# Kernel tuning notes

Measured on AMD Instinct MI355X. Metric: run time of the kernel, lower is better.

## Reference

```python
import jax, jax.numpy as jnp
import numpy as np

B = 4096   # batch
NC = 1     # input channels
K1 = 30    # layer-1 channels
K2 = 80    # layer-2 channels
P = 3      # pooling window (p_x = p_y = 3)
H = 28     # input spatial size (forced: 28 -> conv8 -> 21 -> pool3 -> 7 -> conv4 -> 4)


def _conv(x, w):
    # torch Conv2d (valid, stride 1, no bias): x NCHW, w OIHW
    return jax.lax.conv_general_dilated(x, w, (1, 1), 'VALID',
                                        dimension_numbers=('NCHW', 'OIHW', 'NCHW'))


def _conv_t(x, w):
    # torch ConvTranspose2d (stride 1, no pad, no bias). w: [in, out, kh, kw].
    # Equivalent to full cross-correlation with spatially-flipped, channel-swapped kernel.
    k = w.shape[2]
    wf = jnp.flip(w, (2, 3)).transpose(1, 0, 2, 3)  # -> OIHW
    return jax.lax.conv_general_dilated(x, wf, (1, 1), [(k - 1, k - 1), (k - 1, k - 1)],
                                        dimension_numbers=('NCHW', 'OIHW', 'NCHW'))


def setup_inputs() -> dict:
    key = jax.random.key(0)
    ks = jax.random.split(key, 12)
    sc = 0.05
    f32 = jnp.float32
    return {
        'x':        jax.random.normal(ks[0], (B, NC, H, H), f32),
        'enc1_w':   jax.random.normal(ks[1], (K1, NC, 8, 8), f32) * sc,   # Conv2d OIHW
        'pool_w1':  jax.random.normal(ks[2], (9, 9), f32) * sc,           # Linear [out,in], no bias
        'pool_w2':  jax.random.normal(ks[3], (9, 9), f32) * sc,
        'enc2_w':   jax.random.normal(ks[4], (K2, K1, 4, 4), f32) * sc,
        'h_w':      jax.random.normal(ks[5], (K2, 16, 16), f32) * sc,     # stacked Linear(16,16) [out,in]
        'h_b':      jnp.zeros((K2, 16), f32),
        'mean_w':   jax.random.normal(ks[6], (K2, 16, 16), f32) * sc,
        'mean_b':   jnp.zeros((K2, 16), f32),
        'logvar_w': jax.random.normal(ks[7], (K2, 16, 16), f32) * sc,
        'logvar_b': jnp.zeros((K2, 16), f32),
        'dec2_w':   jax.random.normal(ks[8], (K2, K1, 4, 4), f32) * sc,   # ConvTranspose [in,out,kh,kw]
        'dec1_w':   jax.random.normal(ks[9], (K1, NC, 8, 8), f32) * sc,
        'alpha':    jnp.asarray(0.5, f32),
    }


def reference(x, enc1_w, pool_w1, pool_w2, enc2_w, h_w, h_b,
              mean_w, mean_b, logvar_w, logvar_b, dec2_w, dec1_w, alpha):
    k_pool, k_unpool, k_code, k_noise = jax.random.split(jax.random.key(42), 4)

    # --- encoder conv 1 ---
    c1 = _conv(x, enc1_w)                               # [B, K1, 21, 21]
    b, c, hp, wp = c1.shape
    n, m = hp // P, wp // P                             # 7, 7

    # --- stochastic pooling (vectorized over B, K1, n, m tiles) ---
    tiles = c1.reshape(b, c, n, P, m, P).transpose(0, 1, 2, 4, 3, 5)
    tiles = tiles.reshape(b, c, n, m, P * P)            # [B,K1,7,7,9]
    h1 = jnp.tanh(jnp.einsum('bcnmt,ot->bcnmo', tiles, pool_w1))
    eta = jax.nn.softmax(jnp.einsum('bcnmt,ot->bcnmo', h1, pool_w2), axis=-1)
    zeta = jax.random.categorical(k_pool, jnp.log(eta))  # [B,K1,7,7]
    pooled = jnp.take_along_axis(tiles, zeta[..., None], axis=-1)[..., 0]  # [B,K1,7,7]

    # --- encoder conv 2 + per-channel code MLPs ---
    c2 = _conv(pooled, enc2_w)                          # [B, K2, 4, 4]
    flat = c2.reshape(b, K2, 16)                        # [B, K2, 16]
    h = jnp.tanh(jnp.einsum('bki,koi->bko', flat, h_w) + h_b)
    mean = jnp.einsum('bki,koi->bko', h, mean_w) + mean_b      # [B,K2,16]
    log_var = jnp.einsum('bki,koi->bko', h, logvar_w) + logvar_b

    # --- reparameterized sample per channel ---
    std = jnp.exp(0.5 * log_var)
    s = (mean + std * jax.random.normal(k_code, mean.shape, mean.dtype)).reshape(c2.shape)

    # --- decoder ---
    s2 = _conv_t(s, dec2_w)                             # [B, K1, 7, 7]

    # stochastic unpooling: fresh multinomial draw from the same etas, scatter into tile
    zeta2 = jax.random.categorical(k_unpool, jnp.log(eta))      # [B,K1,7,7]
    tiles_u = jax.nn.one_hot(zeta2, P * P, dtype=s2.dtype) * s2[..., None]  # [B,K1,7,7,9]
    s1 = tiles_u.reshape(b, c, n, m, P, P).transpose(0, 1, 2, 4, 3, 5).reshape(b, c, n * P, m * P)
    s1 = _conv_t(s1, dec1_w)                            # [B, NC, 28, 28]

    # --- add_noise: std = (1/alpha) * eye(H, W), zero std off-diagonal ---
    noise_std = (1.0 / alpha) * jnp.eye(s1.shape[-2], s1.shape[-1], dtype=s1.dtype)
    x_rec = s1 + noise_std * jax.random.normal(k_noise, s1.shape, s1.dtype)

    return x_rec, mean, log_var, eta
```

## Files before the change

kernel.cpp:

```cpp
#include <hip/hip_runtime.h>
#include <cstdint>


#define OFF_MEAN 3211264
#define OFF_LV   8454144
#define OFF_ETA  13697024

constexpr uint64_t ctf(uint32_t k0, uint32_t k1, uint32_t x0, uint32_t x1) {
  uint32_t ks0 = k0, ks1 = k1, ks2 = k0 ^ k1 ^ 0x1BD11BDAu;
  const int rotA[4] = {13, 15, 26, 6};
  const int rotB[4] = {17, 29, 16, 24};
  x0 += ks0; x1 += ks1;
  for (int g = 0; g < 5; ++g) {
    for (int i = 0; i < 4; ++i) {
      int r = (g & 1) ? rotB[i] : rotA[i];
      x0 += x1;
      x1 = (uint32_t)((x1 << r) | (x1 >> (32 - r)));
      x1 ^= x0;
    }
    uint32_t ka = (g + 1) % 3 == 0 ? ks0 : ((g + 1) % 3 == 1 ? ks1 : ks2);
    uint32_t kb = (g + 2) % 3 == 0 ? ks0 : ((g + 2) % 3 == 1 ? ks1 : ks2);
    x0 += ka;
    x1 += kb + (uint32_t)(g + 1);
  }
  return ((uint64_t)x0 << 32) | (uint64_t)x1;
}

constexpr uint64_t KP_ = ctf(0u, 42u, 0u, 0u);
constexpr uint64_t KU_ = ctf(0u, 42u, 0u, 1u);
constexpr uint64_t KC_ = ctf(0u, 42u, 0u, 2u);
constexpr uint64_t KN_ = ctf(0u, 42u, 0u, 3u);
constexpr uint32_t KPOOL0 = (uint32_t)(KP_ >> 32), KPOOL1 = (uint32_t)KP_;
constexpr uint32_t KUNP0  = (uint32_t)(KU_ >> 32), KUNP1  = (uint32_t)KU_;
constexpr uint32_t KCODE0 = (uint32_t)(KC_ >> 32), KCODE1 = (uint32_t)KC_;
constexpr uint32_t KNOIS0 = (uint32_t)(KN_ >> 32), KNOIS1 = (uint32_t)KN_;

__device__ __forceinline__ uint2 tf_dev(uint32_t k0, uint32_t k1, uint32_t x0, uint32_t x1) {
  uint32_t ks2 = k0 ^ k1 ^ 0x1BD11BDAu;
  x0 += k0; x1 += k1;
#define TFR(r) { x0 += x1; x1 = (x1 << (r)) | (x1 >> (32 - (r))); x1 ^= x0; }
  TFR(13) TFR(15) TFR(26) TFR(6)
  x0 += k1;  x1 += ks2 + 1u;
  TFR(17) TFR(29) TFR(16) TFR(24)
  x0 += ks2; x1 += k0 + 2u;
  TFR(13) TFR(15) TFR(26) TFR(6)
  x0 += k0;  x1 += k1 + 3u;
  TFR(17) TFR(29) TFR(16) TFR(24)
  x0 += k1;  x1 += ks2 + 4u;
  TFR(13) TFR(15) TFR(26) TFR(6)
  x0 += ks2; x1 += k0 + 5u;
#undef TFR
  return make_uint2(x0, x1);
}

__device__ __forceinline__ uint32_t rbits32(uint32_t k0, uint32_t k1, uint32_t idx) {
  uint2 r = tf_dev(k0, k1, 0u, idx);
  return r.x ^ r.y;
}

__device__ __forceinline__ float u01_from_bits(uint32_t bits) {
  return __uint_as_float((bits >> 9) | 0x3F800000u) - 1.0f;
}

__device__ __forceinline__ float gumbel_draw(uint32_t k0, uint32_t k1, uint32_t idx) {
  float u01 = u01_from_bits(rbits32(k0, k1, idx));
  float u = fmaxf(__fadd_rn(u01, 1.17549435e-38f), 1.17549435e-38f);
  return -logf(-logf(u));
}

__device__ __forceinline__ float erfinv_xla(float x) {
  float t = __fmul_rn(x, x);
  float w = -log1pf(-t);
  float p;
  if (w < 5.0f) {
    w = __fadd_rn(w, -2.5f);
    p = 2.81022636e-08f;
    p = __fadd_rn(__fmul_rn(p, w), 3.43273939e-07f);
    p = __fadd_rn(__fmul_rn(p, w), -3.5233877e-06f);
    p = __fadd_rn(__fmul_rn(p, w), -4.39150654e-06f);
    p = __fadd_rn(__fmul_rn(p, w), 0.00021858087f);
    p = __fadd_rn(__fmul_rn(p, w), -0.00125372503f);
    p = __fadd_rn(__fmul_rn(p, w), -0.00417768164f);
    p = __fadd_rn(__fmul_rn(p, w), 0.246640727f);
    p = __fadd_rn(__fmul_rn(p, w), 1.50140941f);
  } else {
    w = __fadd_rn(sqrtf(w), -3.0f);
    p = -0.000200214257f;
    p = __fadd_rn(__fmul_rn(p, w), 0.000100950558f);
    p = __fadd_rn(__fmul_rn(p, w), 0.00134934322f);
    p = __fadd_rn(__fmul_rn(p, w), -0.00367342844f);
    p = __fadd_rn(__fmul_rn(p, w), 0.00573950773f);
    p = __fadd_rn(__fmul_rn(p, w), -0.0076224613f);
    p = __fadd_rn(__fmul_rn(p, w), 0.00943887047f);
    p = __fadd_rn(__fmul_rn(p, w), 1.00167406f);
    p = __fadd_rn(__fmul_rn(p, w), 2.83297682f);
  }
  return __fmul_rn(p, x);
}

__device__ __forceinline__ float normal_draw(uint32_t k0, uint32_t k1, uint32_t idx) {
  float u01 = u01_from_bits(rbits32(k0, k1, idx));
  float u = fmaxf(__fadd_rn(__fmul_rn(u01, 2.0f), -0.99999994f), -0.99999994f);
  return __fmul_rn(1.41421356237309515f, erfinv_xla(u));
}

__device__ __forceinline__ float tanh_xla(float x) {
  float ax = fabsf(x);
  float xc = fmaxf(fminf(x, 7.90531110763549805f), -7.90531110763549805f);
  float x2 = __fmul_rn(xc, xc);
  float p = __fmaf_rn(x2, -2.76076847742355e-16f, 2.00018790482477e-13f);
  p = __fmaf_rn(x2, p, -8.60467152213735e-11f);
  p = __fmaf_rn(x2, p, 5.12229709037114e-08f);
  p = __fmaf_rn(x2, p, 1.48572235717979e-05f);
  p = __fmaf_rn(x2, p, 6.37261928875436e-04f);
  p = __fmaf_rn(x2, p, 4.89352455891786e-03f);
  p = __fmul_rn(xc, p);
  float q = __fmaf_rn(x2, 1.19825839466702e-06f, 1.18534705686654e-04f);
  q = __fmaf_rn(x2, q, 2.26843463243900e-03f);
  q = __fmaf_rn(x2, q, 4.89352518554385e-03f);
  return (ax < 0.0004f) ? x : __fdiv_rn(p, q);
}

__global__ __launch_bounds__(256) void k_enc(
    const float* __restrict__ x, const float* __restrict__ enc1_w,
    const float* __restrict__ pw1, const float* __restrict__ pw2,
    const float* __restrict__ enc2_w, const float* __restrict__ h_w,
    const float* __restrict__ h_b, const float* __restrict__ mean_w,
    const float* __restrict__ mean_b, const float* __restrict__ lv_w,
    const float* __restrict__ lv_b,
    float* __restrict__ o_mean, float* __restrict__ o_lv, float* __restrict__ o_eta,
    float* __restrict__ ws_s, unsigned char* __restrict__ ws_z) {
  __shared__ float lds[2866];
  __shared__ float pooled[1470];
  const int b = blockIdx.x, tid = threadIdx.x;

  float* xs  = lds;
  float* w1s = lds + 784;
  float* pp1 = lds + 2704;
  float* pp2 = lds + 2785;
  for (int i = tid; i < 784; i += 256) xs[i] = x[(size_t)b * 784 + i];
  for (int i = tid; i < 1920; i += 256) w1s[i] = enc1_w[i];
  if (tid < 81) { pp1[tid] = pw1[tid]; pp2[tid] = pw2[tid]; }
  __syncthreads();

  for (int g = tid; g < 1470; g += 256) {
    const int c = g / 49, cell = g - c * 49;
    const int n = cell / 7, m = cell - n * 7;
    const int yb = n * 3, xb = m * 3;
    const float* wc = &w1s[c * 64];

    float R[3][10];
#pragma unroll
    for (int rr = 0; rr < 3; ++rr)
#pragma unroll
      for (int i = 0; i < 10; ++i) R[rr][i] = xs[(yb + rr) * 28 + xb + i];

    float tile[9];
#pragma unroll
    for (int i = 0; i < 9; ++i) tile[i] = 0.f;

#pragma unroll
    for (int dy = 0; dy < 8; ++dy) {
      float4 wa = *(const float4*)&wc[dy * 8];
      float4 wb = *(const float4*)&wc[dy * 8 + 4];
      float w8[8] = {wa.x, wa.y, wa.z, wa.w, wb.x, wb.y, wb.z, wb.w};
#pragma unroll
      for (int dx = 0; dx < 8; ++dx) {
        float w = w8[dx];
#pragma unroll
        for (int p = 0; p < 3; ++p)
#pragma unroll
          for (int q = 0; q < 3; ++q)
            tile[p * 3 + q] = __fmaf_rn(R[(dy + p) % 3][dx + q], w, tile[p * 3 + q]);
      }
      if (dy < 7) {
#pragma unroll
        for (int i = 0; i < 10; ++i) R[dy % 3][i] = xs[(yb + dy + 3) * 28 + xb + i];
      }
    }

    float h1v[9];
#pragma unroll
    for (int o = 0; o < 9; ++o) {
      float a = 0.f;
#pragma unroll
      for (int t = 0; t < 9; ++t) a += tile[t] * pp1[o * 9 + t];
      h1v[o] = tanh_xla(a);
    }
    float lg[9], mx = -3.4e38f;
#pragma unroll
    for (int o = 0; o < 9; ++o) {
      float a = 0.f;
#pragma unroll
      for (int t = 0; t < 9; ++t) a += h1v[t] * pp2[o * 9 + t];
      lg[o] = a;
      mx = fmaxf(mx, a);
    }
    float ev[9], ssum = 0.f;
#pragma unroll
    for (int o = 0; o < 9; ++o) { ev[o] = expf(__fadd_rn(lg[o], -mx)); ssum += ev[o]; }
    float leta[9];
    size_t ebase = ((size_t)(b * 30 + c) * 49 + cell) * 9;
#pragma unroll
    for (int o = 0; o < 9; ++o) {
      float e = __fdiv_rn(ev[o], ssum);
      o_eta[ebase + o] = e;
      leta[o] = logf(e);
    }
    uint32_t fb = (uint32_t)ebase;
    float best1 = -3.4e38f, best2 = -3.4e38f, pooledv = 0.f;
    int z2 = 0;
#pragma unroll
    for (int t = 0; t < 9; ++t) {
      float v1 = __fadd_rn(leta[t], gumbel_draw(KPOOL0, KPOOL1, fb + t));
      bool t1 = v1 > best1; best1 = t1 ? v1 : best1; pooledv = t1 ? tile[t] : pooledv;
      float v2 = __fadd_rn(leta[t], gumbel_draw(KUNP0, KUNP1, fb + t));
      bool t2 = v2 > best2; best2 = t2 ? v2 : best2; z2 = t2 ? t : z2;
    }
    pooled[g] = pooledv;
    ws_z[(size_t)b * 1470 + g] = (unsigned char)z2;
  }
  __syncthreads();

  float* c2s = lds;
  float* hs  = lds + 1280;
  const int k2l = tid >> 4, pos = tid & 15;
  const int uy = pos >> 2, ux = pos & 3;
  {
    float acc[5] = {0.f, 0.f, 0.f, 0.f, 0.f};
    for (int c = 0; c < 30; ++c) {
      float pr[16];
#pragma unroll
      for (int dy = 0; dy < 4; ++dy)
#pragma unroll
        for (int dx = 0; dx < 4; ++dx)
          pr[dy * 4 + dx] = pooled[c * 49 + (uy + dy) * 7 + ux + dx];
#pragma unroll
      for (int j = 0; j < 5; ++j) {
        const float4* wr = (const float4*)&enc2_w[(size_t)((j * 16 + k2l) * 30 + c) * 16];
        float4 w0 = wr[0], w1 = wr[1], w2 = wr[2], w3 = wr[3];
        float a = acc[j];
        a = __fmaf_rn(pr[0],  w0.x, a);  a = __fmaf_rn(pr[1],  w0.y, a);
        a = __fmaf_rn(pr[2],  w0.z, a);  a = __fmaf_rn(pr[3],  w0.w, a);
        a = __fmaf_rn(pr[4],  w1.x, a);  a = __fmaf_rn(pr[5],  w1.y, a);
        a = __fmaf_rn(pr[6],  w1.z, a);  a = __fmaf_rn(pr[7],  w1.w, a);
        a = __fmaf_rn(pr[8],  w2.x, a);  a = __fmaf_rn(pr[9],  w2.y, a);
        a = __fmaf_rn(pr[10], w2.z, a);  a = __fmaf_rn(pr[11], w2.w, a);
        a = __fmaf_rn(pr[12], w3.x, a);  a = __fmaf_rn(pr[13], w3.y, a);
        a = __fmaf_rn(pr[14], w3.z, a);  a = __fmaf_rn(pr[15], w3.w, a);
        acc[j] = a;
      }
    }
#pragma unroll
    for (int j = 0; j < 5; ++j) c2s[(j * 16 + k2l) * 16 + pos] = acc[j];
  }
  __syncthreads();

#pragma unroll
  for (int j = 0; j < 5; ++j) {
    int it = tid + j * 256;
    int k2 = it >> 4;
    const float4* wr4 = (const float4*)&h_w[(size_t)it * 16];
    float4 a0 = wr4[0], a1 = wr4[1], a2 = wr4[2], a3 = wr4[3];
    float wv16[16] = {a0.x, a0.y, a0.z, a0.w, a1.x, a1.y, a1.z, a1.w,
                      a2.x, a2.y, a2.z, a2.w, a3.x, a3.y, a3.z, a3.w};
    float d = 0.f;
#pragma unroll
    for (int i = 0; i < 16; ++i) d += c2s[k2 * 16 + i] * wv16[i];
    hs[it] = tanh_xla(__fadd_rn(d, h_b[it]));
  }
  __syncthreads();

#pragma unroll
  for (int j = 0; j < 5; ++j) {
    int it = tid + j * 256;
    int k2 = it >> 4;
    const float4* wm4 = (const float4*)&mean_w[(size_t)it * 16];
    const float4* wl4 = (const float4*)&lv_w[(size_t)it * 16];
    float4 m0 = wm4[0], m1 = wm4[1], m2 = wm4[2], m3 = wm4[3];
    float4 l0 = wl4[0], l1 = wl4[1], l2 = wl4[2], l3 = wl4[3];
    float wm16[16] = {m0.x, m0.y, m0.z, m0.w, m1.x, m1.y, m1.z, m1.w,
                      m2.x, m2.y, m2.z, m2.w, m3.x, m3.y, m3.z, m3.w};
    float wl16[16] = {l0.x, l0.y, l0.z, l0.w, l1.x, l1.y, l1.z, l1.w,
                      l2.x, l2.y, l2.z, l2.w, l3.x, l3.y, l3.z, l3.w};
    float dm = 0.f, dl = 0.f;
#pragma unroll
    for (int i = 0; i < 16; ++i) {
      float hv = hs[k2 * 16 + i];
      dm += hv * wm16[i];
      dl += hv * wl16[i];
    }
    float mean = __fadd_rn(dm, mean_b[it]);
    float lv = __fadd_rn(dl, lv_b[it]);
    size_t gi = (size_t)b * 1280 + it;
    o_mean[gi] = mean;
    o_lv[gi] = lv;
    float stdv = expf(__fmul_rn(0.5f, lv));
    float z = normal_draw(KCODE0, KCODE1, (uint32_t)(b * 1280 + it));
    ws_s[gi] = __fadd_rn(mean, __fmul_rn(stdv, z));
  }
}

__global__ __launch_bounds__(256) void k_expand(const float* __restrict__ dec2_w,
                                                float* __restrict__ Wexp) {
  int idx = blockIdx.x * 256 + threadIdx.x;
  int k = idx / 1472, t = idx - k * 1472;
  int k2 = k >> 4, iy = (k >> 2) & 3, ix = k & 3;
  int c = t / 49, cell = t - c * 49;
  int u = cell / 7, v = cell - u * 7;
  int du = u - iy, dv = v - ix;
  float val = 0.f;
  if (t < 1470 && (unsigned)du < 4u && (unsigned)dv < 4u)
    val = dec2_w[((k2 * 30 + c) << 4) + (du << 2) + dv];
  Wexp[idx] = val;
}

__global__ __launch_bounds__(256) void k_gemm(const float* __restrict__ A,
                                              const float* __restrict__ Bm,
                                              float* __restrict__ C) {
  __shared__ float As[16][132];
  __shared__ float Bs[16][64];
  const int tid = threadIdx.x;
  const int n0 = blockIdx.x * 64;
  const int m0 = blockIdx.y * 128;
  const int tx = tid & 15, ty = tid >> 4;

  float acc[8][4];
#pragma unroll
  for (int i = 0; i < 8; ++i)
#pragma unroll
    for (int j = 0; j < 4; ++j) acc[i][j] = 0.f;

  const int fa_r0 = tid >> 2, fa_c = (tid & 3) << 2;
  const int fb_k = tid >> 4, fb_c = (tid & 15) << 2;

  for (int k0 = 0; k0 < 1280; k0 += 16) {
    __syncthreads();
    float4 a0 = *(const float4*)&A[(size_t)(m0 + fa_r0) * 1280 + k0 + fa_c];
    float4 a1 = *(const float4*)&A[(size_t)(m0 + 64 + fa_r0) * 1280 + k0 + fa_c];
    float4 bv = *(const float4*)&Bm[(size_t)(k0 + fb_k) * 1472 + n0 + fb_c];
    As[fa_c + 0][fa_r0] = a0.x;  As[fa_c + 1][fa_r0] = a0.y;
    As[fa_c + 2][fa_r0] = a0.z;  As[fa_c + 3][fa_r0] = a0.w;
    As[fa_c + 0][64 + fa_r0] = a1.x;  As[fa_c + 1][64 + fa_r0] = a1.y;
    As[fa_c + 2][64 + fa_r0] = a1.z;  As[fa_c + 3][64 + fa_r0] = a1.w;
    *(float4*)&Bs[fb_k][fb_c] = bv;
    __syncthreads();

#pragma unroll
    for (int kk = 0; kk < 16; ++kk) {
      float4 av0 = *(const float4*)&As[kk][ty * 8];
      float4 av1 = *(const float4*)&As[kk][ty * 8 + 4];
      float4 bv0 = *(const float4*)&Bs[kk][tx * 4];
      float am[8] = {av0.x, av0.y, av0.z, av0.w, av1.x, av1.y, av1.z, av1.w};
      float bn[4] = {bv0.x, bv0.y, bv0.z, bv0.w};
#pragma unroll
      for (int i = 0; i < 8; ++i)
#pragma unroll
        for (int j = 0; j < 4; ++j) acc[i][j] = __fmaf_rn(am[i], bn[j], acc[i][j]);
    }
  }

#pragma unroll
  for (int i = 0; i < 8; ++i) {
    size_t row = (size_t)(m0 + ty * 8 + i);
    float4 o = make_float4(acc[i][0], acc[i][1], acc[i][2], acc[i][3]);
    *(float4*)&C[row * 1472 + n0 + tx * 4] = o;
  }
}

__global__ __launch_bounds__(256) void k_unpool(
    const float* __restrict__ S2, const unsigned char* __restrict__ ws_z,
    const float* __restrict__ dec1_w, const float* __restrict__ alpha,
    float* __restrict__ o_xrec) {
  __shared__ float w1s[1920];
  __shared__ float2 tv[1470];
  const int b = blockIdx.x, tid = threadIdx.x;

  for (int i = tid; i < 1920; i += 256) w1s[i] = dec1_w[i];
#pragma unroll
  for (int j = 0; j < 6; ++j) {
    int t = tid + j * 256;
    if (t < 1470) {
      int c = t / 49, cell = t - c * 49;
      int n = cell / 7, m = cell - n * 7;
      int z = ws_z[(size_t)b * 1470 + t];
      int p = z / 3, q = z - p * 3;
      float val = S2[(size_t)b * 1472 + t];
      tv[t] = make_float2(val, __uint_as_float((uint32_t)((n * 3 + p) | ((m * 3 + q) << 8))));
    }
  }
  __syncthreads();

  float inva = __fdiv_rn(1.0f, alpha[0]);
  for (int pix = tid; pix < 784; pix += 256) {
    int y = pix / 28, x = pix - y * 28;
    int nlo = (y >= 9) ? ((y - 9 + 2) / 3) : 0;
    int nhi = min(6, y / 3);
    int mlo = (x >= 9) ? ((x - 9 + 2) / 3) : 0;
    int mhi = min(6, x / 3);

    float acc = 0.f;
    for (int c = 0; c < 30; ++c) {
      const float2* tvc = &tv[c * 49];
      const float* wc = &w1s[c * 64];
#pragma unroll
      for (int dn = 0; dn < 4; ++dn) {
        int n = nlo + dn;
        bool nok = n <= nhi;
        int nn = nok ? n : nhi;
#pragma unroll
        for (int dm = 0; dm < 4; ++dm) {
          int m = mlo + dm;
          bool ok = nok && (m <= mhi);
          int mm = (m <= mhi) ? m : mhi;
          float2 tvv = tvc[nn * 7 + mm];
          uint32_t pp = __float_as_uint(tvv.y);
          int dy = y - (int)(pp & 0xffu);
          int dx = x - (int)(pp >> 8);
          ok = ok && ((unsigned)dy < 8u) && ((unsigned)dx < 8u);
          float wvv = wc[((dy & 7) << 3) + (dx & 7)];
          acc = __fmaf_rn(ok ? tvv.x : 0.f, wvv, acc);
        }
      }
    }
    if (y == x) {
      float zn = normal_draw(KNOIS0, KNOIS1, (uint32_t)(b * 784 + pix));
      acc = __fadd_rn(acc, __fmul_rn(inva, zn));
    }
    o_xrec[(size_t)b * 784 + pix] = acc;
  }
}

extern "C" void kernel_launch(void* const* d_in, const int* in_sizes, int n_in,
                              void* d_out, int out_size, void* d_ws, size_t ws_size,
                              hipStream_t stream) {
  const float* x      = (const float*)d_in[0];
  const float* enc1_w = (const float*)d_in[1];
  const float* pw1    = (const float*)d_in[2];
  const float* pw2    = (const float*)d_in[3];
  const float* enc2_w = (const float*)d_in[4];
  const float* h_w    = (const float*)d_in[5];
  const float* h_b    = (const float*)d_in[6];
  const float* mean_w = (const float*)d_in[7];
  const float* mean_b = (const float*)d_in[8];
  const float* lv_w   = (const float*)d_in[9];
  const float* lv_b   = (const float*)d_in[10];
  const float* dec2_w = (const float*)d_in[11];
  const float* dec1_w = (const float*)d_in[12];
  const float* alpha  = (const float*)d_in[13];

  float* out = (float*)d_out;
  float* o_xrec = out;
  float* o_mean = out + OFF_MEAN;
  float* o_lv   = out + OFF_LV;
  float* o_eta  = out + OFF_ETA;

  char* wsb = (char*)d_ws;
  float* ws_s = (float*)wsb;
  unsigned char* ws_z = (unsigned char*)(wsb + 20971520);
  float* Wexp = (float*)(wsb + 26992640);
  float* S2   = (float*)(wsb + 34529280);

  k_expand<<<dim3(7360), dim3(256), 0, stream>>>(dec2_w, Wexp);
  k_enc<<<dim3(4096), dim3(256), 0, stream>>>(
      x, enc1_w, pw1, pw2, enc2_w, h_w, h_b, mean_w, mean_b, lv_w, lv_b,
      o_mean, o_lv, o_eta, ws_s, ws_z);
  k_gemm<<<dim3(23, 32), dim3(256), 0, stream>>>(ws_s, Wexp, S2);
  k_unpool<<<dim3(4096), dim3(256), 0, stream>>>(S2, ws_z, dec1_w, alpha, o_xrec);
}
```

Measured before the change: 1.690 ms.

## Retile decoder GEMM with register prefetch and process two images per unpool block

The decoder GEMM tile changes from 128x64 to 64x128, with clamped loads and a guarded store for the ragged N edge. It also prefetches the next K slice into registers while computing the current one, so global load latency overlaps the FMAs. The unpool kernel now handles two batch images per block, which amortizes the dec1 weight staging and gives each thread more pixels to work on. The trade-offs are more shared memory per unpool block and wasted work on the padded final GEMM column tile.

```diff
diff --git a/kernel.cpp b/kernel.cpp
--- a/kernel.cpp
+++ b/kernel.cpp
@@ -318,53 +318,68 @@
 __global__ __launch_bounds__(256) void k_gemm(const float* __restrict__ A,
                                               const float* __restrict__ Bm,
                                               float* __restrict__ C) {
-  __shared__ float As[16][132];
-  __shared__ float Bs[16][64];
+  __shared__ float As[16][68];
+  __shared__ float Bs[16][128];
   const int tid = threadIdx.x;
-  const int n0 = blockIdx.x * 64;
-  const int m0 = blockIdx.y * 128;
+  const int n0 = blockIdx.x * 128;
+  const int m0 = blockIdx.y * 64;
   const int tx = tid & 15, ty = tid >> 4;
 
-  float acc[8][4];
-#pragma unroll
-  for (int i = 0; i < 8; ++i)
-#pragma unroll
-    for (int j = 0; j < 4; ++j) acc[i][j] = 0.f;
-
-  const int fa_r0 = tid >> 2, fa_c = (tid & 3) << 2;
-  const int fb_k = tid >> 4, fb_c = (tid & 15) << 2;
+  float acc[4][8];
+#pragma unroll
+  for (int i = 0; i < 4; ++i)
+#pragma unroll
+    for (int j = 0; j < 8; ++j) acc[i][j] = 0.f;
+
+  const int a_r = tid >> 2, a_c = (tid & 3) << 2;
+  const int b_k = tid >> 4, b_c = (tid & 15) << 3;
+  const int bcol = n0 + b_c;
+  const int bcol_c = (bcol > 1464) ? 1464 : bcol;
+
+  const float* pa = &A[(size_t)(m0 + a_r) * 1280 + a_c];
+  const float* pb = &Bm[(size_t)b_k * 1472 + bcol_c];
+
+  float4 av = *(const float4*)pa;
+  float4 bv0 = *(const float4*)pb;
+  float4 bv1 = *(const float4*)(pb + 4);
 
   for (int k0 = 0; k0 < 1280; k0 += 16) {
     __syncthreads();
-    float4 a0 = *(const float4*)&A[(size_t)(m0 + fa_r0) * 1280 + k0 + fa_c];
-    float4 a1 = *(const float4*)&A[(size_t)(m0 + 64 + fa_r0) * 1280 + k0 + fa_c];
-    float4 bv = *(const float4*)&Bm[(size_t)(k0 + fb_k) * 1472 + n0 + fb_c];
-    As[fa_c + 0][fa_r0] = a0.x;  As[fa_c + 1][fa_r0] = a0.y;
-    As[fa_c + 2][fa_r0] = a0.z;  As[fa_c + 3][fa_r0] = a0.w;
-    As[fa_c + 0][64 + fa_r0] = a1.x;  As[fa_c + 1][64 + fa_r0] = a1.y;
-    As[fa_c + 2][64 + fa_r0] = a1.z;  As[fa_c + 3][64 + fa_r0] = a1.w;
-    *(float4*)&Bs[fb_k][fb_c] = bv;
+    As[a_c + 0][a_r] = av.x;  As[a_c + 1][a_r] = av.y;
+    As[a_c + 2][a_r] = av.z;  As[a_c + 3][a_r] = av.w;
+    *(float4*)&Bs[b_k][b_c] = bv0;
+    *(float4*)&Bs[b_k][b_c + 4] = bv1;
     __syncthreads();
 
+    if (k0 + 16 < 1280) {
+      av = *(const float4*)(pa + k0 + 16);
+      bv0 = *(const float4*)(pb + (size_t)(k0 + 16) * 1472);
+      bv1 = *(const float4*)(pb + (size_t)(k0 + 16) * 1472 + 4);
+    }
+
 #pragma unroll
     for (int kk = 0; kk < 16; ++kk) {
-      float4 av0 = *(const float4*)&As[kk][ty * 8];
-      float4 av1 = *(const float4*)&As[kk][ty * 8 + 4];
-      float4 bv0 = *(const float4*)&Bs[kk][tx * 4];
-      float am[8] = {av0.x, av0.y, av0.z, av0.w, av1.x, av1.y, av1.z, av1.w};
-      float bn[4] = {bv0.x, bv0.y, bv0.z, bv0.w};
-#pragma unroll
-      for (int i = 0; i < 8; ++i)
-#pragma unroll
-        for (int j = 0; j < 4; ++j) acc[i][j] = __fmaf_rn(am[i], bn[j], acc[i][j]);
-    }
-  }
-
-#pragma unroll
-  for (int i = 0; i < 8; ++i) {
-    size_t row = (size_t)(m0 + ty * 8 + i);
-    float4 o = make_float4(acc[i][0], acc[i][1], acc[i][2], acc[i][3]);
-    *(float4*)&C[row * 1472 + n0 + tx * 4] = o;
+      float4 a4 = *(const float4*)&As[kk][ty * 4];
+      float4 b4a = *(const float4*)&Bs[kk][tx * 8];
+      float4 b4b = *(const float4*)&Bs[kk][tx * 8 + 4];
+      float am[4] = {a4.x, a4.y, a4.z, a4.w};
+      float bn[8] = {b4a.x, b4a.y, b4a.z, b4a.w, b4b.x, b4b.y, b4b.z, b4b.w};
+#pragma unroll
+      for (int i = 0; i < 4; ++i)
+#pragma unroll
+        for (int j = 0; j < 8; ++j) acc[i][j] = __fmaf_rn(am[i], bn[j], acc[i][j]);
+    }
+  }
+
+  if (n0 + tx * 8 < 1472) {
+#pragma unroll
+    for (int i = 0; i < 4; ++i) {
+      size_t row = (size_t)(m0 + ty * 4 + i);
+      float4 o0 = make_float4(acc[i][0], acc[i][1], acc[i][2], acc[i][3]);
+      float4 o1 = make_float4(acc[i][4], acc[i][5], acc[i][6], acc[i][7]);
+      *(float4*)&C[row * 1472 + n0 + tx * 8] = o0;
+      *(float4*)&C[row * 1472 + n0 + tx * 8 + 4] = o1;
+    }
   }
 }
 
@@ -373,35 +388,38 @@
     const float* __restrict__ dec1_w, const float* __restrict__ alpha,
     float* __restrict__ o_xrec) {
   __shared__ float w1s[1920];
-  __shared__ float2 tv[1470];
-  const int b = blockIdx.x, tid = threadIdx.x;
+  __shared__ float2 tv[2][1470];
+  const int b0 = blockIdx.x * 2, tid = threadIdx.x;
 
   for (int i = tid; i < 1920; i += 256) w1s[i] = dec1_w[i];
-#pragma unroll
-  for (int j = 0; j < 6; ++j) {
-    int t = tid + j * 256;
-    if (t < 1470) {
-      int c = t / 49, cell = t - c * 49;
-      int n = cell / 7, m = cell - n * 7;
-      int z = ws_z[(size_t)b * 1470 + t];
-      int p = z / 3, q = z - p * 3;
-      float val = S2[(size_t)b * 1472 + t];
-      tv[t] = make_float2(val, __uint_as_float((uint32_t)((n * 3 + p) | ((m * 3 + q) << 8))));
-    }
+  for (int t = tid; t < 2940; t += 256) {
+    int bb = t >= 1470;
+    int tt = t - bb * 1470;
+    int c = tt / 49, cell = tt - c * 49;
+    int n = cell / 7, m = cell - n * 7;
+    int b = b0 + bb;
+    int z = ws_z[(size_t)b * 1470 + tt];
+    int p = z / 3, q = z - p * 3;
+    float val = S2[(size_t)b * 1472 + tt];
+    tv[bb][tt] = make_float2(val, __uint_as_float((uint32_t)((n * 3 + p) | ((m * 3 + q) << 8))));
   }
   __syncthreads();
 
   float inva = __fdiv_rn(1.0f, alpha[0]);
-  for (int pix = tid; pix < 784; pix += 256) {
-    int y = pix / 28, x = pix - y * 28;
+  for (int pix = tid; pix < 1568; pix += 256) {
+    int bb = pix >= 784;
+    int p2 = pix - bb * 784;
+    int b = b0 + bb;
+    int y = p2 / 28, x = p2 - y * 28;
     int nlo = (y >= 9) ? ((y - 9 + 2) / 3) : 0;
     int nhi = min(6, y / 3);
     int mlo = (x >= 9) ? ((x - 9 + 2) / 3) : 0;
     int mhi = min(6, x / 3);
 
     float acc = 0.f;
+    const float2* tvb = tv[bb];
     for (int c = 0; c < 30; ++c) {
-      const float2* tvc = &tv[c * 49];
+      const float2* tvc = &tvb[c * 49];
       const float* wc = &w1s[c * 64];
 #pragma unroll
       for (int dn = 0; dn < 4; ++dn) {
@@ -424,10 +442,10 @@
       }
     }
     if (y == x) {
-      float zn = normal_draw(KNOIS0, KNOIS1, (uint32_t)(b * 784 + pix));
+      float zn = normal_draw(KNOIS0, KNOIS1, (uint32_t)(b * 784 + p2));
       acc = __fadd_rn(acc, __fmul_rn(inva, zn));
     }
-    o_xrec[(size_t)b * 784 + pix] = acc;
+    o_xrec[(size_t)b * 784 + p2] = acc;
   }
 }
 
@@ -465,6 +483,6 @@
   k_enc<<<dim3(4096), dim3(256), 0, stream>>>(
       x, enc1_w, pw1, pw2, enc2_w, h_w, h_b, mean_w, mean_b, lv_w, lv_b,
       o_mean, o_lv, o_eta, ws_s, ws_z);
-  k_gemm<<<dim3(23, 32), dim3(256), 0, stream>>>(ws_s, Wexp, S2);
-  k_unpool<<<dim3(4096), dim3(256), 0, stream>>>(S2, ws_z, dec1_w, alpha, o_xrec);
-}
+  k_gemm<<<dim3(12, 64), dim3(256), 0, stream>>>(ws_s, Wexp, S2);
+  k_unpool<<<dim3(2048), dim3(256), 0, stream>>>(S2, ws_z, dec1_w, alpha, o_xrec);
+}
```

New measurement: 1.646 ms. 2.6% less time.
